# Kernel optimization log

Measured on AMD Instinct MI355X. Metric: run time of the kernel, lower is better.

## Reference

```python
import jax, jax.numpy as jnp
import numpy as np

N_HEAD = 6


def setup_inputs() -> dict:
    key = jax.random.key(0)
    k1, k2, k3 = jax.random.split(key, 3)
    B, N, D = 16, 512, 768
    d_head = D // N_HEAD
    p_mask = jnp.ones((B, N), dtype=jnp.float32)
    feature = jax.random.normal(k1, (B, N, D), dtype=jnp.float32)
    # nn.Linear weights (out, in); scaled like torch default init
    W = jax.random.normal(k2, (D, D), dtype=jnp.float32) / np.sqrt(D)
    # attn Linear(2*d_head -> n_head); only the diagonal head rows are used
    Wa = jax.random.normal(k3, (N_HEAD, 2 * d_head), dtype=jnp.float32) / np.sqrt(2 * d_head)
    return {"p_mask": p_mask, "feature": feature, "W": W, "Wa": Wa, "num_layers": 2}


def reference(p_mask, feature, W, Wa, num_layers):
    B, N, D = feature.shape
    H = N_HEAD
    Dh = D // H
    # adj[b,q,k] = p_mask[b,q] * p_mask[b,k]  (bmm of unsqueezed mask)
    adj = p_mask[:, :, None] * p_mask[:, None, :]  # (B,N,N)
    mask = adj[:, :, :, None] > 0                   # (B,N,N,1)
    for _ in range(num_layers):
        residual = feature
        qk = (feature @ W.T).reshape(B, N, H, Dh)  # (B,N,H,Dh)
        # concat(q,k) @ Wa[h] decomposes into query part + key part
        sq = jnp.einsum('bqhd,hd->bqh', qk, Wa[:, :Dh])
        sk = jnp.einsum('bkhd,hd->bkh', qk, Wa[:, Dh:])
        score = jnp.tanh(sq[:, :, None, :] + sk[:, None, :, :])  # (B,N,N,H)
        # masked_fill with -1e-8 where adj == 0 (faithful to source)
        score = jnp.where(mask, score, jnp.float32(-1e-8))
        attn = jax.nn.softmax(score, axis=2)  # softmax over key dim (dim=-2)
        # dropout p=0 in eval -> identity
        hid = jnp.tanh(jnp.einsum('bqkh,bkhd->bqhd', attn, qk))  # (B,N,H,Dh)
        feature = residual + hid.reshape(B, N, D)
    return feature
```

## Files before the change

kernel.cpp:

```cpp
#include <hip/hip_runtime.h>
#include <hip/hip_bf16.h>
#include <stdint.h>

#define BATCH 16
#define NSEQ  512
#define DMODEL 768
#define NHEAD 6
#define DHEAD 128
#define MROWS (BATCH * NSEQ)
#define QBLK  32
#define KTILE 64

typedef __attribute__((ext_vector_type(8))) __bf16 bf16x8;
typedef __attribute__((ext_vector_type(4))) __bf16 bf16x4;
typedef __attribute__((ext_vector_type(4))) float  f32x4;
typedef __attribute__((ext_vector_type(4))) unsigned int u32x4;

#define GLD16(gp, lp) __builtin_amdgcn_global_load_lds( \
    (const __attribute__((address_space(1))) unsigned int*)(gp), \
    (__attribute__((address_space(3))) unsigned int*)(lp), 16, 0, 0)

#define BAR_PLAIN() do { asm volatile("" ::: "memory"); \
    __builtin_amdgcn_s_barrier(); asm volatile("" ::: "memory"); } while (0)
#define BAR_LGKM() do { asm volatile("s_waitcnt lgkmcnt(0)" ::: "memory"); \
    __builtin_amdgcn_s_barrier(); asm volatile("" ::: "memory"); } while (0)

__global__ void cvt_bf16_dual(const float* __restrict__ srcA, __bf16* __restrict__ dstA, int n4A,
                              const float* __restrict__ srcB, __bf16* __restrict__ dstB, int n4B) {
    int i = blockIdx.x * blockDim.x + threadIdx.x;
    const float* s;
    __bf16* d;
    int idx;
    if (i < n4A) { s = srcA; d = dstA; idx = i; }
    else         { idx = i - n4A; if (idx >= n4B) return; s = srcB; d = dstB; }
    float4 v = reinterpret_cast<const float4*>(s)[idx];
    bf16x4 o;
    o.x = (__bf16)v.x; o.y = (__bf16)v.y; o.z = (__bf16)v.z; o.w = (__bf16)v.w;
    reinterpret_cast<bf16x4*>(d)[idx] = o;
}

__global__ __launch_bounds__(256) void gemm_bt(const __bf16* __restrict__ A,
                                               const __bf16* __restrict__ Bm,
                                               __bf16* __restrict__ C,
                                               const float* __restrict__ Wa,
                                               const float* __restrict__ pmask,
                                               float* __restrict__ eq_t,
                                               float* __restrict__ ek_t) {
    __shared__ __align__(16) __bf16 As[2][64 * 32];
    __shared__ __align__(16) __bf16 Bs[2][128 * 32];
    const int tid  = threadIdx.x;
    const int lane = tid & 63;
    const int wave = tid >> 6;
    const int wm = wave >> 1, wn = wave & 1;

    const int wg  = blockIdx.x;
    const int nid = (wg & 7) * 96 + (wg >> 3);
    const int bx  = nid % 6;
    const int by  = nid / 6;
    const int m0 = by * 64;
    const int n0 = bx * 128;

    f32x4 acc[2][4] = {};

    const int e0   = tid * 8;
    const int row0 = tid >> 2;
    const int k0i  = (tid & 3) * 8;

    const int lr = lane & 15;
    const int lg = lane >> 4;
    const int kb = lg * 8;

    #define STAGE(kt, bufi) do { \
        GLD16(A  + (size_t)(m0 + row0)      * DMODEL + (kt) + k0i, &As[bufi][e0]); \
        GLD16(Bm + (size_t)(n0 + row0)      * DMODEL + (kt) + k0i, &Bs[bufi][e0]); \
        GLD16(Bm + (size_t)(n0 + row0 + 64) * DMODEL + (kt) + k0i, &Bs[bufi][e0 + 2048]); \
    } while (0)

    STAGE(0, 0);

    for (int t = 0; t < 24; t++) {
        const int buf = t & 1;
        if (t < 23) {
            STAGE((t + 1) * 32, buf ^ 1);
            asm volatile("s_waitcnt vmcnt(3)" ::: "memory");
        } else {
            asm volatile("s_waitcnt vmcnt(0)" ::: "memory");
        }
        __builtin_amdgcn_s_barrier();
        asm volatile("" ::: "memory");

        bf16x8 af[2], bfv[4];
        #pragma unroll
        for (int i = 0; i < 2; i++)
            af[i] = *reinterpret_cast<const bf16x8*>(&As[buf][(wm * 32 + i * 16 + lr) * 32 + kb]);
        #pragma unroll
        for (int j = 0; j < 4; j++)
            bfv[j] = *reinterpret_cast<const bf16x8*>(&Bs[buf][(wn * 64 + j * 16 + lr) * 32 + kb]);
        #pragma unroll
        for (int i = 0; i < 2; i++)
            #pragma unroll
            for (int j = 0; j < 4; j++)
                acc[i][j] = __builtin_amdgcn_mfma_f32_16x16x32_bf16(af[i], bfv[j], acc[i][j], 0, 0, 0);

        BAR_PLAIN();
    }
    #undef STAGE

    const int rg = lg * 4;
    #pragma unroll
    for (int i = 0; i < 2; i++) {
        #pragma unroll
        for (int j = 0; j < 4; j++) {
            #pragma unroll
            for (int r = 0; r < 4; r++) {
                int row = m0 + wm * 32 + i * 16 + rg + r;
                int col = n0 + wn * 64 + j * 16 + lr;
                C[(size_t)row * DMODEL + col] = (__bf16)acc[i][j][r];
            }
        }
    }

    const int h = bx;
    float wqv[4], wkv[4];
    #pragma unroll
    for (int j = 0; j < 4; j++) {
        int d = wn * 64 + j * 16 + lr;
        wqv[j] = Wa[h * 256 + d];
        wkv[j] = Wa[h * 256 + 128 + d];
    }
    float* red = reinterpret_cast<float*>(&As[0][0]);
    #pragma unroll
    for (int i = 0; i < 2; i++) {
        #pragma unroll
        for (int r = 0; r < 4; r++) {
            float aq = 0.f, ak = 0.f;
            #pragma unroll
            for (int j = 0; j < 4; j++) {
                aq += acc[i][j][r] * wqv[j];
                ak += acc[i][j][r] * wkv[j];
            }
            #pragma unroll
            for (int off = 1; off < 16; off <<= 1) {
                aq += __shfl_xor(aq, off);
                ak += __shfl_xor(ak, off);
            }
            if (lr == 0) {
                int row = wm * 32 + i * 16 + rg + r;
                red[(0 * 64 + row) * 2 + wn] = aq;
                red[(1 * 64 + row) * 2 + wn] = ak;
            }
        }
    }
    __syncthreads();
    if (tid < 64) {
        int row = m0 + tid;
        float s = red[tid * 2] + red[tid * 2 + 1];
        eq_t[(size_t)h * MROWS + row] = (pmask[row] > 0.f) ? __expf(2.f * s) : 0.f;
    } else if (tid < 128) {
        int rl  = tid - 64;
        int row = m0 + rl;
        float s = red[(64 + rl) * 2] + red[(64 + rl) * 2 + 1];
        ek_t[(size_t)h * MROWS + row] = (pmask[row] > 0.f) ? __expf(2.f * s) : 0.f;
    }
}

template<int LAYER>
__global__ __launch_bounds__(256) void attn_pv(const __bf16* __restrict__ QK,
                                               const float* __restrict__ eq_t,
                                               const float* __restrict__ ek_t,
                                               const float* __restrict__ resf,
                                               const __bf16* __restrict__ resb,
                                               float* __restrict__ outf,
                                               __bf16* __restrict__ outb) {
    const int wg  = blockIdx.x;
    const int nid = (wg & 7) * 192 + (wg >> 3);
    const int qt = nid & 15;
    const int hb = nid >> 4;
    const int h  = hb % NHEAD;
    const int b  = hb / NHEAD;
    const int q0 = qt * QBLK;

    __shared__ __align__(16) __bf16 w[QBLK][512];
    __shared__ __align__(16) __bf16 Vt[2][DHEAD * KTILE];
    const int tid  = threadIdx.x;
    const int lane = tid & 63;
    const int wave = tid >> 6;

    const int wd0 = wave * 32;
    const int lr  = lane & 15;
    const int lg  = lane >> 4;

    const int sd0 = (tid & 15) * 8;
    const int sk0 = (tid >> 4) * 4;
    const __bf16* Vbase = QK + (size_t)b * NSEQ * DMODEL + (size_t)h * DHEAD + sd0;

    u32x4 A0, A1, A2, A3, B0, B1, B2, B3;
    #define LOADS(S0, S1, S2, S3, t) do { \
        const __bf16* p = Vbase + (size_t)((t) * KTILE + sk0) * DMODEL; \
        S0 = *reinterpret_cast<const u32x4*>(p); \
        S1 = *reinterpret_cast<const u32x4*>(p + DMODEL); \
        S2 = *reinterpret_cast<const u32x4*>(p + 2 * DMODEL); \
        S3 = *reinterpret_cast<const u32x4*>(p + 3 * DMODEL); \
    } while (0)
    #define WRITEV(S0, S1, S2, S3, bufi) do { \
        char* vtw = reinterpret_cast<char*>(&Vt[bufi][0]); \
        _Pragma("unroll") \
        for (int j = 0; j < 8; j++) { \
            int d = sd0 + j; \
            int swz = j ^ (tid & 7); \
            unsigned sel = (j & 1) ? 0x07060302u : 0x05040100u; \
            unsigned lo = __builtin_amdgcn_perm(S1[j >> 1], S0[j >> 1], sel); \
            unsigned hi = __builtin_amdgcn_perm(S3[j >> 1], S2[j >> 1], sel); \
            unsigned long long pk = (unsigned long long)lo | ((unsigned long long)hi << 32); \
            *reinterpret_cast<unsigned long long*>(vtw + d * 128 + ((sk0 ^ (swz << 3)) * 2)) = pk; \
        } \
    } while (0)

    LOADS(A0, A1, A2, A3, 0);
    LOADS(B0, B1, B2, B3, 1);

    float res[2][4][2];
    #pragma unroll
    for (int qh = 0; qh < 2; qh++) {
        #pragma unroll
        for (int r = 0; r < 4; r++) {
            int ql = qh * 16 + lg * 4 + r;
            #pragma unroll
            for (int n = 0; n < 2; n++) {
                int d = wd0 + n * 16 + lr;
                size_t o = ((size_t)(b * NSEQ + q0 + ql)) * DMODEL + (size_t)h * DHEAD + d;
                if constexpr (LAYER == 0) res[qh][r][n] = resf[o];
                else                      res[qh][r][n] = (float)resb[o];
            }
        }
    }

    const int k0 = lane * 8;
    const size_t sbase = (size_t)h * MROWS + b * NSEQ;
    float4 e0v = *reinterpret_cast<const float4*>(&ek_t[sbase + k0]);
    float4 e1v = *reinterpret_cast<const float4*>(&ek_t[sbase + k0 + 4]);
    float ek[8] = {e0v.x, e0v.y, e0v.z, e0v.w, e1v.x, e1v.y, e1v.z, e1v.w};
    float eq[8];
    #pragma unroll
    for (int g = 0; g < 8; g++)
        eq[g] = eq_t[sbase + q0 + wave * 8 + g];

    WRITEV(A0, A1, A2, A3, 0);
    LOADS(A0, A1, A2, A3, 2);

    #pragma unroll
    for (int g = 0; g < 8; g++) {
        int q = wave * 8 + g;
        float eqv = eq[g];
        bf16x8 wv;
        #pragma unroll
        for (int j = 0; j < 8; j++) {
            float u = eqv * ek[j];
            float z = __builtin_amdgcn_rcpf(u + 1.f);
            float p = __expf(fmaf(z, -2.f, 1.f));
            wv[j] = (__bf16)(u > 0.f ? p : 1.0f);
        }
        *reinterpret_cast<bf16x8*>(&w[q][k0 ^ ((q & 7) << 3)]) = wv;
    }
    BAR_LGKM();

    bf16x8 vones;
    #pragma unroll
    for (int e = 0; e < 8; e++) vones[e] = (__bf16)1.0f;

    f32x4 acc[2][2] = {};
    f32x4 accs[2] = {};

    const int wswz = (lr & 7) << 3;

    #pragma unroll
    for (int t = 0; t < 8; t++) {
        const int buf = t & 1;
        const char* vtr = reinterpret_cast<const char*>(&Vt[buf][0]);
        if (t < 7) {
            if ((t & 1) == 0) WRITEV(B0, B1, B2, B3, buf ^ 1);
            else              WRITEV(A0, A1, A2, A3, buf ^ 1);
        }
        if (t < 5) {
            if ((t & 1) == 0) LOADS(B0, B1, B2, B3, t + 3);
            else              LOADS(A0, A1, A2, A3, t + 3);
        }
        __builtin_amdgcn_s_setprio(1);
        #pragma unroll
        for (int ks = 0; ks < 2; ks++) {
            int cb = (t * 64 + ks * 32 + lg * 8) ^ wswz;
            bf16x8 af0 = *reinterpret_cast<const bf16x8*>(&w[lr][cb]);
            bf16x8 af1 = *reinterpret_cast<const bf16x8*>(&w[16 + lr][cb]);
            #pragma unroll
            for (int n = 0; n < 2; n++) {
                int d    = wd0 + n * 16 + lr;
                int kbk  = ks * 4 + lg;
                int swzd = (d & 7) ^ ((d >> 3) & 7);
                bf16x8 bv = *reinterpret_cast<const bf16x8*>(vtr + d * 128 + ((kbk ^ swzd) << 4));
                acc[0][n] = __builtin_amdgcn_mfma_f32_16x16x32_bf16(af0, bv, acc[0][n], 0, 0, 0);
                acc[1][n] = __builtin_amdgcn_mfma_f32_16x16x32_bf16(af1, bv, acc[1][n], 0, 0, 0);
            }
            accs[0] = __builtin_amdgcn_mfma_f32_16x16x32_bf16(af0, vones, accs[0], 0, 0, 0);
            accs[1] = __builtin_amdgcn_mfma_f32_16x16x32_bf16(af1, vones, accs[1], 0, 0, 0);
        }
        __builtin_amdgcn_s_setprio(0);
        if (t < 7) BAR_LGKM();
    }

    #pragma unroll
    for (int qh = 0; qh < 2; qh++) {
        #pragma unroll
        for (int r = 0; r < 4; r++) {
            int ql = qh * 16 + lg * 4 + r;
            float rden = __builtin_amdgcn_rcpf(accs[qh][r]);
            #pragma unroll
            for (int n = 0; n < 2; n++) {
                int d  = wd0 + n * 16 + lr;
                float hv = acc[qh][n][r] * rden;
                float e2 = __expf(2.f * hv);
                float tv = 1.f - 2.f * __builtin_amdgcn_rcpf(e2 + 1.f);
                size_t o = ((size_t)(b * NSEQ + q0 + ql)) * DMODEL + (size_t)h * DHEAD + d;
                float ov = res[qh][r][n] + tv;
                if constexpr (LAYER == 0) outb[o] = (__bf16)ov;
                else                      outf[o] = ov;
            }
        }
    }
    #undef LOADS
    #undef WRITEV
}

extern "C" void kernel_launch(void* const* d_in, const int* in_sizes, int n_in,
                              void* d_out, int out_size, void* d_ws, size_t ws_size,
                              hipStream_t stream) {
    const float* pmask   = (const float*)d_in[0];
    const float* feature = (const float*)d_in[1];
    const float* W       = (const float*)d_in[2];
    const float* Wa      = (const float*)d_in[3];
    float* out = (float*)d_out;
    char* ws = (char*)d_ws;

    __bf16* Abf  = (__bf16*)ws;
    __bf16* Wbf  = (__bf16*)(ws + 12582912);
    __bf16* QKbf = (__bf16*)(ws + 12582912 + 1179648);
    float*  eq   = (float*)(ws + 12582912 + 1179648 + 12582912);
    float*  ek   = eq + MROWS * NHEAD;

    const int wN4    = (DMODEL * DMODEL) / 4;
    const int featN4 = (MROWS * DMODEL) / 4;

    hipLaunchKernelGGL(cvt_bf16_dual, dim3((wN4 + featN4 + 255) / 256), dim3(256), 0, stream,
                       W, Wbf, wN4, feature, Abf, featN4);

    hipLaunchKernelGGL(gemm_bt, dim3(768), dim3(256), 0, stream,
                       Abf, Wbf, QKbf, Wa, pmask, eq, ek);
    hipLaunchKernelGGL((attn_pv<0>), dim3(1536), dim3(256), 0, stream,
                       QKbf, eq, ek, feature, (const __bf16*)nullptr,
                       (float*)nullptr, Abf);

    hipLaunchKernelGGL(gemm_bt, dim3(768), dim3(256), 0, stream,
                       Abf, Wbf, QKbf, Wa, pmask, eq, ek);
    hipLaunchKernelGGL((attn_pv<1>), dim3(1536), dim3(256), 0, stream,
                       QKbf, eq, ek, (const float*)nullptr, Abf,
                       out, (__bf16*)nullptr);
}
```

Baseline: 103.5 us.

## Fuse fp32-to-bf16 feature conversion into first GEMM and reorder attention prefetch

The first projection GEMM now loads fp32 feature rows directly into a swizzled LDS tile and converts them to bf16 while building MFMA fragments. The separate pass that converted the whole feature tensor to bf16 is dropped, leaving only the weight conversion kernel. This removes one full read and write of the activation tensor, but doubles the A-tile LDS footprint and global load volume inside the first GEMM. Separately, the attention kernel moves its V-tile writes and next-tile loads after the MFMA block instead of before it, changing how memory and compute overlap.

Result: no change. 103.7 us (+0.2%).

```diff
diff --git a/kernel.cpp b/kernel.cpp
--- a/kernel.cpp
+++ b/kernel.cpp
@@ -25,28 +25,29 @@
 #define BAR_LGKM() do { asm volatile("s_waitcnt lgkmcnt(0)" ::: "memory"); \
     __builtin_amdgcn_s_barrier(); asm volatile("" ::: "memory"); } while (0)
 
-__global__ void cvt_bf16_dual(const float* __restrict__ srcA, __bf16* __restrict__ dstA, int n4A,
-                              const float* __restrict__ srcB, __bf16* __restrict__ dstB, int n4B) {
+__global__ void cvt_bf16_kernel(const float* __restrict__ src,
+                                __bf16* __restrict__ dst, int n4) {
     int i = blockIdx.x * blockDim.x + threadIdx.x;
-    const float* s;
-    __bf16* d;
-    int idx;
-    if (i < n4A) { s = srcA; d = dstA; idx = i; }
-    else         { idx = i - n4A; if (idx >= n4B) return; s = srcB; d = dstB; }
-    float4 v = reinterpret_cast<const float4*>(s)[idx];
-    bf16x4 o;
-    o.x = (__bf16)v.x; o.y = (__bf16)v.y; o.z = (__bf16)v.z; o.w = (__bf16)v.w;
-    reinterpret_cast<bf16x4*>(d)[idx] = o;
+    if (i < n4) {
+        float4 v = reinterpret_cast<const float4*>(src)[i];
+        bf16x4 o;
+        o.x = (__bf16)v.x; o.y = (__bf16)v.y; o.z = (__bf16)v.z; o.w = (__bf16)v.w;
+        reinterpret_cast<bf16x4*>(dst)[i] = o;
+    }
 }
 
-__global__ __launch_bounds__(256) void gemm_bt(const __bf16* __restrict__ A,
+template<bool AFP32>
+__global__ __launch_bounds__(256) void gemm_bt(const void* __restrict__ Av,
                                                const __bf16* __restrict__ Bm,
                                                __bf16* __restrict__ C,
                                                const float* __restrict__ Wa,
                                                const float* __restrict__ pmask,
                                                float* __restrict__ eq_t,
                                                float* __restrict__ ek_t) {
-    __shared__ __align__(16) __bf16 As[2][64 * 32];
+    const __bf16* Ab = reinterpret_cast<const __bf16*>(Av);
+    const float*  Af = reinterpret_cast<const float*>(Av);
+
+    __shared__ __align__(16) __bf16 As[2][AFP32 ? 4096 : 2048];
     __shared__ __align__(16) __bf16 Bs[2][128 * 32];
     const int tid  = threadIdx.x;
     const int lane = tid & 63;
@@ -70,11 +71,22 @@
     const int lg = lane >> 4;
     const int kb = lg * 8;
 
-    #define STAGE(kt, bufi) do { \
-        GLD16(A  + (size_t)(m0 + row0)      * DMODEL + (kt) + k0i, &As[bufi][e0]); \
-        GLD16(Bm + (size_t)(n0 + row0)      * DMODEL + (kt) + k0i, &Bs[bufi][e0]); \
-        GLD16(Bm + (size_t)(n0 + row0 + 64) * DMODEL + (kt) + k0i, &Bs[bufi][e0 + 2048]); \
-    } while (0)
+    auto STAGE = [&](int kt, int bufi) {
+        if constexpr (AFP32) {
+            #pragma unroll
+            for (int i2 = 0; i2 < 2; i2++) {
+                int tt  = tid + 256 * i2;
+                int row = tt >> 3;
+                int k0s = ((tt & 7) * 4) ^ ((row & 7) << 2);
+                GLD16(Af + (size_t)(m0 + row) * DMODEL + kt + k0s,
+                      reinterpret_cast<float*>(&As[bufi][0]) + tt * 4);
+            }
+        } else {
+            GLD16(Ab + (size_t)(m0 + row0) * DMODEL + kt + k0i, &As[bufi][e0]);
+        }
+        GLD16(Bm + (size_t)(n0 + row0)      * DMODEL + kt + k0i, &Bs[bufi][e0]);
+        GLD16(Bm + (size_t)(n0 + row0 + 64) * DMODEL + kt + k0i, &Bs[bufi][e0 + 2048]);
+    };
 
     STAGE(0, 0);
 
@@ -82,7 +94,8 @@
         const int buf = t & 1;
         if (t < 23) {
             STAGE((t + 1) * 32, buf ^ 1);
-            asm volatile("s_waitcnt vmcnt(3)" ::: "memory");
+            if constexpr (AFP32) asm volatile("s_waitcnt vmcnt(4)" ::: "memory");
+            else                 asm volatile("s_waitcnt vmcnt(3)" ::: "memory");
         } else {
             asm volatile("s_waitcnt vmcnt(0)" ::: "memory");
         }
@@ -90,9 +103,25 @@
         asm volatile("" ::: "memory");
 
         bf16x8 af[2], bfv[4];
-        #pragma unroll
-        for (int i = 0; i < 2; i++)
-            af[i] = *reinterpret_cast<const bf16x8*>(&As[buf][(wm * 32 + i * 16 + lr) * 32 + kb]);
+        if constexpr (AFP32) {
+            const float* A32 = reinterpret_cast<const float*>(&As[buf][0]);
+            const int sw = (lr & 7) << 2;
+            #pragma unroll
+            for (int i = 0; i < 2; i++) {
+                int row = wm * 32 + i * 16 + lr;
+                f32x4 lo = *reinterpret_cast<const f32x4*>(&A32[row * 32 + (kb ^ sw)]);
+                f32x4 hi = *reinterpret_cast<const f32x4*>(&A32[row * 32 + ((kb + 4) ^ sw)]);
+                #pragma unroll
+                for (int j = 0; j < 4; j++) {
+                    af[i][j]     = (__bf16)lo[j];
+                    af[i][4 + j] = (__bf16)hi[j];
+                }
+            }
+        } else {
+            #pragma unroll
+            for (int i = 0; i < 2; i++)
+                af[i] = *reinterpret_cast<const bf16x8*>(&As[buf][(wm * 32 + i * 16 + lr) * 32 + kb]);
+        }
         #pragma unroll
         for (int j = 0; j < 4; j++)
             bfv[j] = *reinterpret_cast<const bf16x8*>(&Bs[buf][(wn * 64 + j * 16 + lr) * 32 + kb]);
@@ -104,7 +133,6 @@
 
         BAR_PLAIN();
     }
-    #undef STAGE
 
     const int rg = lg * 4;
     #pragma unroll
@@ -277,14 +305,6 @@
     for (int t = 0; t < 8; t++) {
         const int buf = t & 1;
         const char* vtr = reinterpret_cast<const char*>(&Vt[buf][0]);
-        if (t < 7) {
-            if ((t & 1) == 0) WRITEV(B0, B1, B2, B3, buf ^ 1);
-            else              WRITEV(A0, A1, A2, A3, buf ^ 1);
-        }
-        if (t < 5) {
-            if ((t & 1) == 0) LOADS(B0, B1, B2, B3, t + 3);
-            else              LOADS(A0, A1, A2, A3, t + 3);
-        }
         __builtin_amdgcn_s_setprio(1);
         #pragma unroll
         for (int ks = 0; ks < 2; ks++) {
@@ -304,6 +324,14 @@
             accs[1] = __builtin_amdgcn_mfma_f32_16x16x32_bf16(af1, vones, accs[1], 0, 0, 0);
         }
         __builtin_amdgcn_s_setprio(0);
+        if (t < 7) {
+            if ((t & 1) == 0) WRITEV(B0, B1, B2, B3, buf ^ 1);
+            else              WRITEV(A0, A1, A2, A3, buf ^ 1);
+        }
+        if (t < 5) {
+            if ((t & 1) == 0) LOADS(B0, B1, B2, B3, t + 3);
+            else              LOADS(A0, A1, A2, A3, t + 3);
+        }
         if (t < 7) BAR_LGKM();
     }
 
@@ -346,20 +374,19 @@
     float*  eq   = (float*)(ws + 12582912 + 1179648 + 12582912);
     float*  ek   = eq + MROWS * NHEAD;
 
-    const int wN4    = (DMODEL * DMODEL) / 4;
-    const int featN4 = (MROWS * DMODEL) / 4;
-
-    hipLaunchKernelGGL(cvt_bf16_dual, dim3((wN4 + featN4 + 255) / 256), dim3(256), 0, stream,
-                       W, Wbf, wN4, feature, Abf, featN4);
-
-    hipLaunchKernelGGL(gemm_bt, dim3(768), dim3(256), 0, stream,
-                       Abf, Wbf, QKbf, Wa, pmask, eq, ek);
+    const int wN4 = (DMODEL * DMODEL) / 4;
+
+    hipLaunchKernelGGL(cvt_bf16_kernel, dim3((wN4 + 255) / 256), dim3(256), 0, stream,
+                       W, Wbf, wN4);
+
+    hipLaunchKernelGGL((gemm_bt<true>), dim3(768), dim3(256), 0, stream,
+                       (const void*)feature, Wbf, QKbf, Wa, pmask, eq, ek);
     hipLaunchKernelGGL((attn_pv<0>), dim3(1536), dim3(256), 0, stream,
                        QKbf, eq, ek, feature, (const __bf16*)nullptr,
                        (float*)nullptr, Abf);
 
-    hipLaunchKernelGGL(gemm_bt, dim3(768), dim3(256), 0, stream,
-                       Abf, Wbf, QKbf, Wa, pmask, eq, ek);
+    hipLaunchKernelGGL((gemm_bt<false>), dim3(768), dim3(256), 0, stream,
+                       (const void*)Abf, Wbf, QKbf, Wa, pmask, eq, ek);
     hipLaunchKernelGGL((attn_pv<1>), dim3(1536), dim3(256), 0, stream,
                        QKbf, eq, ek, (const float*)nullptr, Abf,
                        out, (__bf16*)nullptr);
```
